# Optimization experiments

Measured on AMD Instinct MI355X. Metric: run time of the kernel, lower is better.

Reference implementation:

```python
import jax, jax.numpy as jnp
import numpy as np

N_NODES = 100000
N_EDGES = 3200000


def gcn_conv(x, W, b, row, col, n):
    # PyG GCNConv: add self-loops, symmetric normalization D^-1/2 (A+I) D^-1/2 (X W) + b
    xw = x @ W  # [N, out]
    loops = jnp.arange(n)
    row2 = jnp.concatenate([row, loops])
    col2 = jnp.concatenate([col, loops])
    deg = jax.ops.segment_sum(jnp.ones_like(col2, dtype=xw.dtype), col2, num_segments=n)
    dinv = jnp.where(deg > 0, jax.lax.rsqrt(deg), 0.0)
    norm = dinv[row2] * dinv[col2]  # [E+N]
    msg = xw[row2] * norm[:, None]  # gather + scale
    out = jax.ops.segment_sum(msg, col2, num_segments=n)  # scatter-add to targets
    return out + b


def setup_inputs() -> dict:
    key = jax.random.key(0)
    ks = jax.random.split(key, 9)
    x = jax.random.normal(ks[0], (N_NODES, 2), dtype=jnp.float32)
    edge_index = jax.random.randint(ks[1], (2, N_EDGES), 0, N_NODES, dtype=jnp.int64)
    edge_attr = jax.random.normal(ks[2], (N_EDGES, 1), dtype=jnp.float32)
    # params (glorot-ish scale)
    W1 = jax.random.normal(ks[3], (2, 16), dtype=jnp.float32) * (1.0 / np.sqrt(2))
    b1 = jnp.zeros((16,), dtype=jnp.float32)
    We = jax.random.normal(ks[4], (33, 4), dtype=jnp.float32) * (1.0 / np.sqrt(33))
    be = jnp.zeros((4,), dtype=jnp.float32)
    W2 = jax.random.normal(ks[5], (16, 2), dtype=jnp.float32) * (1.0 / np.sqrt(16))
    b2 = jnp.zeros((2,), dtype=jnp.float32)
    return {"x": x, "edge_index": edge_index, "edge_attr": edge_attr,
            "W1": W1, "b1": b1, "We": We, "be": be, "W2": W2, "b2": b2}


def reference(x, edge_index, edge_attr, W1, b1, We, be, W2, b2):
    row, col = edge_index[0], edge_index[1]
    n = x.shape[0]
    h = gcn_conv(x, W1, b1, row, col, n)  # [N, 16]
    # edge update: gather src/dst features, concat with edge_attr, Linear+ReLU
    e_in = jnp.concatenate([h[row], edge_attr, h[col]], axis=1)  # [E, 33]
    e_out = jax.nn.relu(e_in @ We + be)  # [E, 4]
    out_x = gcn_conv(h, W2, b2, row, col, n)  # [N, 2]
    return jax.nn.log_softmax(out_x, axis=1), jax.nn.log_softmax(e_out, axis=1)
```

## Files before the change

kernel.cpp:

```cpp
#include <hip/hip_runtime.h>


#define BLK 256
#define BLKP 1024
#define CH 12500
#define VIT ((CH + 4 * BLKP - 1) / (4 * BLKP))
#define BSH 7
#define BSZ 128
#define NBMAX 1024
#define PAD 16
#define S1 262144.0f
#define S2 65536.0f
#define BIAS 8388608

__global__ __launch_bounds__(BLKP) void k_hist(const int* __restrict__ col,
                                               int* __restrict__ gcount,
                                               int E, int NB) {
    __shared__ int hist[NBMAX];
    int t = threadIdx.x;
    if (t < NBMAX) hist[t] = 0;
    __syncthreads();
    int e0 = blockIdx.x * CH;
    int cnt = min(CH, E - e0);
    #pragma unroll
    for (int i = 0; i < VIT; i++) {
        int k = 4 * (t + i * BLKP);
        if (k + 3 < cnt) {
            int4 c = *reinterpret_cast<const int4*>(col + e0 + k);
            atomicAdd(&hist[c.x >> BSH], 1);
            atomicAdd(&hist[c.y >> BSH], 1);
            atomicAdd(&hist[c.z >> BSH], 1);
            atomicAdd(&hist[c.w >> BSH], 1);
        } else if (k < cnt) {
            for (int q = k; q < cnt; q++)
                atomicAdd(&hist[col[e0 + q] >> BSH], 1);
        }
    }
    __syncthreads();
    if (t < NB) {
        int h = hist[t];
        if (h) atomicAdd(&gcount[t * PAD], h);
    }
}

__global__ void k_scan(const int* __restrict__ gcount, int* __restrict__ gbase,
                       int* __restrict__ gcursor, int NB) {
    __shared__ int sa[NBMAX], sb[NBMAX];
    int t = threadIdx.x;
    for (int i = t; i < NBMAX; i += BLK) sa[i] = (i < NB) ? gcount[i * PAD] : 0;
    __syncthreads();
    int *src = sa, *dst = sb;
    for (int off = 1; off < NBMAX; off <<= 1) {
        for (int i = t; i < NBMAX; i += BLK)
            dst[i] = src[i] + ((i >= off) ? src[i - off] : 0);
        __syncthreads();
        int* tmp = src; src = dst; dst = tmp;
    }
    for (int i = t; i < NB; i += BLK) {
        int ex = src[i] - gcount[i * PAD];
        gbase[i] = ex;
        gcursor[i * PAD] = ex;
    }
    if (t == 0) gbase[NB] = src[NB - 1];
}

__global__ __launch_bounds__(BLKP) void k_part(const int* __restrict__ row,
                                               const int* __restrict__ col,
                                               int* __restrict__ gcursor,
                                               unsigned* __restrict__ part,
                                               int E, int NB) {
    __shared__ int hist[NBMAX];
    __shared__ int lstart[NBMAX];
    __shared__ int lcur[NBMAX];
    __shared__ int gb[NBMAX];
    __shared__ unsigned sbuf[CH];
    __shared__ unsigned short bid[CH];
    __shared__ int wsum[BLKP / 64];
    int t = threadIdx.x;
    int e0 = blockIdx.x * CH;
    int cnt = min(CH, E - e0);
    if (t < NBMAX) hist[t] = 0;
    __syncthreads();
    int4 cv[VIT];
    #pragma unroll
    for (int i = 0; i < VIT; i++) {
        int k = 4 * (t + i * BLKP);
        if (k + 3 < cnt) {
            int4 c = *reinterpret_cast<const int4*>(col + e0 + k);
            cv[i] = c;
            atomicAdd(&hist[c.x >> BSH], 1);
            atomicAdd(&hist[c.y >> BSH], 1);
            atomicAdd(&hist[c.z >> BSH], 1);
            atomicAdd(&hist[c.w >> BSH], 1);
        } else if (k < cnt) {
            int4 c = make_int4(0, 0, 0, 0);
            int m = cnt - k;
            c.x = col[e0 + k];             atomicAdd(&hist[c.x >> BSH], 1);
            if (m > 1) { c.y = col[e0 + k + 1]; atomicAdd(&hist[c.y >> BSH], 1); }
            if (m > 2) { c.z = col[e0 + k + 2]; atomicAdd(&hist[c.z >> BSH], 1); }
            cv[i] = c;
        }
    }
    __syncthreads();
    int h = hist[t];
    int lane = t & 63, wid = t >> 6;
    int v = h;
    #pragma unroll
    for (int off = 1; off < 64; off <<= 1) {
        int u = __shfl_up(v, off);
        if (lane >= off) v += u;
    }
    if (lane == 63) wsum[wid] = v;
    __syncthreads();
    int base = v - h;
    for (int w = 0; w < wid; w++) base += wsum[w];
    lstart[t] = base;
    lcur[t]   = base;
    gb[t] = h ? atomicAdd(&gcursor[t * PAD], h) : 0;
    __syncthreads();
    #pragma unroll
    for (int i = 0; i < VIT; i++) {
        int k = 4 * (t + i * BLKP);
        if (k + 3 < cnt) {
            int4 r = *reinterpret_cast<const int4*>(row + e0 + k);
            int4 c = cv[i];
            int b0 = c.x >> BSH, b1 = c.y >> BSH, b2 = c.z >> BSH, b3 = c.w >> BSH;
            int o0 = atomicAdd(&lcur[b0], 1);
            int o1 = atomicAdd(&lcur[b1], 1);
            int o2 = atomicAdd(&lcur[b2], 1);
            int o3 = atomicAdd(&lcur[b3], 1);
            sbuf[o0] = ((unsigned)r.x << BSH) | (unsigned)(c.x & (BSZ - 1));
            sbuf[o1] = ((unsigned)r.y << BSH) | (unsigned)(c.y & (BSZ - 1));
            sbuf[o2] = ((unsigned)r.z << BSH) | (unsigned)(c.z & (BSZ - 1));
            sbuf[o3] = ((unsigned)r.w << BSH) | (unsigned)(c.w & (BSZ - 1));
            bid[o0] = (unsigned short)b0;
            bid[o1] = (unsigned short)b1;
            bid[o2] = (unsigned short)b2;
            bid[o3] = (unsigned short)b3;
        } else if (k < cnt) {
            int m = cnt - k;
            int cs[3] = {cv[i].x, cv[i].y, cv[i].z};
            for (int q = 0; q < m && q < 3; q++) {
                int c = cs[q];
                int r = row[e0 + k + q];
                int b = c >> BSH;
                int off = atomicAdd(&lcur[b], 1);
                sbuf[off] = ((unsigned)r << BSH) | (unsigned)(c & (BSZ - 1));
                bid[off] = (unsigned short)b;
            }
        }
    }
    __syncthreads();
    for (int j = t; j < cnt; j += BLKP) {
        int b = bid[j];
        part[gb[b] + (j - lstart[b])] = sbuf[j];
    }
}

__global__ void k_nodeA(const unsigned* __restrict__ part, const int* __restrict__ gbase,
                        const float2* __restrict__ x2, float* __restrict__ dinv,
                        int* __restrict__ degi, int2* __restrict__ pi, int N) {
    __shared__ int cnt[BSZ];
    int t = threadIdx.x;
    if (t < BSZ) cnt[t] = 0;
    __syncthreads();
    int b = blockIdx.x;
    int j0 = gbase[b], j1 = gbase[b + 1];
    for (int j = j0 + 4 * t; j < j1; j += 4 * BLK) {
        int m = j1 - j;
        if (m >= 4) {
            unsigned w0 = part[j], w1 = part[j + 1], w2 = part[j + 2], w3 = part[j + 3];
            atomicAdd(&cnt[w0 & (BSZ - 1)], 1);
            atomicAdd(&cnt[w1 & (BSZ - 1)], 1);
            atomicAdd(&cnt[w2 & (BSZ - 1)], 1);
            atomicAdd(&cnt[w3 & (BSZ - 1)], 1);
        } else {
            for (int q = 0; q < m; q++)
                atomicAdd(&cnt[part[j + q] & (BSZ - 1)], 1);
        }
    }
    __syncthreads();
    if (t < BSZ) {
        int node = (b << BSH) + t;
        if (node < N) {
            int dg = cnt[t];
            degi[node] = dg;
            float d = rsqrtf((float)(dg + 1));
            dinv[node] = d;
            float2 xv = x2[node];
            pi[node] = make_int2(__float2int_rn(xv.x * d * S1),
                                 __float2int_rn(xv.y * d * S1));
        }
    }
}

__device__ __forceinline__ unsigned long long packi2(int2 p) {
    return ((unsigned long long)(unsigned)p.x << 32) | (unsigned)(p.y + BIAS);
}

__global__ void k_nodeB(const unsigned* __restrict__ part, const int* __restrict__ gbase,
                        const float* __restrict__ dinv, const int* __restrict__ degi,
                        const int2* __restrict__ pi,
                        const float* __restrict__ W1, const float* __restrict__ b1,
                        const float* __restrict__ W2, const float* __restrict__ We,
                        const float* __restrict__ be,
                        float4* __restrict__ U, float4* __restrict__ V,
                        int2* __restrict__ qi, int N) {
    __shared__ unsigned long long acc[BSZ];
    __shared__ float sW1[32], sb1[16], sW2[32], sWr[64], sWc[64], sbe[4];
    int t = threadIdx.x;
    if (t < BSZ) acc[t] = 0ull;
    if (t < 32) sW1[t] = W1[t];
    else if (t < 64) sW2[t - 32] = W2[t - 32];
    else if (t < 80) sb1[t - 64] = b1[t - 64];
    else if (t < 144) sWr[t - 80] = We[t - 80];
    else if (t < 208) sWc[t - 144] = We[68 + (t - 144)];
    else if (t < 212) sbe[t - 208] = be[t - 208];
    __syncthreads();
    int b = blockIdx.x;
    int j0 = gbase[b], j1 = gbase[b + 1];
    for (int j = j0 + 4 * t; j < j1; j += 4 * BLK) {
        int m = j1 - j;
        if (m >= 4) {
            unsigned w0 = part[j], w1 = part[j + 1], w2 = part[j + 2], w3 = part[j + 3];
            int2 p0 = pi[w0 >> BSH], p1 = pi[w1 >> BSH];
            int2 p2 = pi[w2 >> BSH], p3 = pi[w3 >> BSH];
            atomicAdd(&acc[w0 & (BSZ - 1)], packi2(p0));
            atomicAdd(&acc[w1 & (BSZ - 1)], packi2(p1));
            atomicAdd(&acc[w2 & (BSZ - 1)], packi2(p2));
            atomicAdd(&acc[w3 & (BSZ - 1)], packi2(p3));
        } else {
            for (int q = 0; q < m; q++) {
                unsigned w = part[j + q];
                atomicAdd(&acc[w & (BSZ - 1)], packi2(pi[w >> BSH]));
            }
        }
    }
    __syncthreads();
    if (t < BSZ) {
        int node = (b << BSH) + t;
        if (node < N) {
            unsigned long long a = acc[t];
            int sx = (int)(unsigned)(a >> 32);
            long long sy = (long long)(unsigned)(a & 0xffffffffull)
                         - (long long)degi[node] * BIAS;
            int2 ps = pi[node];
            float d = dinv[node];
            float ax = (float)(ps.x + (long long)sx) * (1.0f / S1);
            float ay = (float)(ps.y + sy) * (1.0f / S1);
            float s0 = d * ax, s1 = d * ay;
            float u0 = sbe[0], u1 = sbe[1], u2 = sbe[2], u3 = sbe[3];
            float v0 = 0.f, v1 = 0.f, v2 = 0.f, v3 = 0.f;
            float w0 = 0.f, w1 = 0.f;
            #pragma unroll
            for (int jj = 0; jj < 16; jj++) {
                float hj = fmaf(s0, sW1[jj], fmaf(s1, sW1[16 + jj], sb1[jj]));
                u0 = fmaf(hj, sWr[4 * jj + 0], u0);
                u1 = fmaf(hj, sWr[4 * jj + 1], u1);
                u2 = fmaf(hj, sWr[4 * jj + 2], u2);
                u3 = fmaf(hj, sWr[4 * jj + 3], u3);
                v0 = fmaf(hj, sWc[4 * jj + 0], v0);
                v1 = fmaf(hj, sWc[4 * jj + 1], v1);
                v2 = fmaf(hj, sWc[4 * jj + 2], v2);
                v3 = fmaf(hj, sWc[4 * jj + 3], v3);
                w0 = fmaf(hj, sW2[2 * jj], w0);
                w1 = fmaf(hj, sW2[2 * jj + 1], w1);
            }
            U[node] = make_float4(u0, u1, u2, u3);
            V[node] = make_float4(v0, v1, v2, v3);
            float qx = w0 * d, qy = w1 * d;
            qi[node] = make_int2(__float2int_rn(qx * S2), __float2int_rn(qy * S2));
        }
    }
}

__device__ __forceinline__ float4 edge_lsm(float4 u, float4 v, float av,
                                           const float* sW16) {
    float a0 = u.x + fmaf(av, sW16[0], v.x);
    float a1 = u.y + fmaf(av, sW16[1], v.y);
    float a2 = u.z + fmaf(av, sW16[2], v.z);
    float a3 = u.w + fmaf(av, sW16[3], v.w);
    a0 = fmaxf(a0, 0.f); a1 = fmaxf(a1, 0.f);
    a2 = fmaxf(a2, 0.f); a3 = fmaxf(a3, 0.f);
    float m = fmaxf(fmaxf(a0, a1), fmaxf(a2, a3));
    float s = expf(a0 - m) + expf(a1 - m) + expf(a2 - m) + expf(a3 - m);
    float l = m + logf(s);
    return make_float4(a0 - l, a1 - l, a2 - l, a3 - l);
}

__global__ void k_edge(const int* __restrict__ row, const int* __restrict__ col,
                       const float* __restrict__ ea, const float4* __restrict__ U,
                       const float4* __restrict__ V, const float* __restrict__ We,
                       float4* __restrict__ eout, int E) {
    __shared__ float sW16[4];
    int t = threadIdx.x;
    if (t < 4) sW16[t] = We[64 + t];
    __syncthreads();
    int base = blockIdx.x * (4 * BLK);
    int e0 = base + t;
    if (base + 4 * BLK <= E) {
        int r0 = row[e0], r1 = row[e0 + BLK], r2 = row[e0 + 2 * BLK], r3 = row[e0 + 3 * BLK];
        int c0 = col[e0], c1 = col[e0 + BLK], c2 = col[e0 + 2 * BLK], c3 = col[e0 + 3 * BLK];
        float a0 = ea[e0], a1 = ea[e0 + BLK], a2 = ea[e0 + 2 * BLK], a3 = ea[e0 + 3 * BLK];
        float4 u0 = U[r0], u1 = U[r1], u2 = U[r2], u3 = U[r3];
        float4 v0 = V[c0], v1 = V[c1], v2 = V[c2], v3 = V[c3];
        eout[e0]           = edge_lsm(u0, v0, a0, sW16);
        eout[e0 + BLK]     = edge_lsm(u1, v1, a1, sW16);
        eout[e0 + 2 * BLK] = edge_lsm(u2, v2, a2, sW16);
        eout[e0 + 3 * BLK] = edge_lsm(u3, v3, a3, sW16);
    } else {
        for (int q = 0; q < 4; q++) {
            int e = e0 + q * BLK;
            if (e < E)
                eout[e] = edge_lsm(U[row[e]], V[col[e]], ea[e], sW16);
        }
    }
}

__global__ void k_nodeC(const unsigned* __restrict__ part, const int* __restrict__ gbase,
                        const float* __restrict__ dinv, const int* __restrict__ degi,
                        const int2* __restrict__ qi,
                        const float* __restrict__ b2, float2* __restrict__ outn, int N) {
    __shared__ unsigned long long acc[BSZ];
    int t = threadIdx.x;
    if (t < BSZ) acc[t] = 0ull;
    __syncthreads();
    int b = blockIdx.x;
    int j0 = gbase[b], j1 = gbase[b + 1];
    for (int j = j0 + 4 * t; j < j1; j += 4 * BLK) {
        int m = j1 - j;
        if (m >= 4) {
            unsigned w0 = part[j], w1 = part[j + 1], w2 = part[j + 2], w3 = part[j + 3];
            int2 q0 = qi[w0 >> BSH], q1 = qi[w1 >> BSH];
            int2 q2 = qi[w2 >> BSH], q3 = qi[w3 >> BSH];
            atomicAdd(&acc[w0 & (BSZ - 1)], packi2(q0));
            atomicAdd(&acc[w1 & (BSZ - 1)], packi2(q1));
            atomicAdd(&acc[w2 & (BSZ - 1)], packi2(q2));
            atomicAdd(&acc[w3 & (BSZ - 1)], packi2(q3));
        } else {
            for (int q = 0; q < m; q++) {
                unsigned w = part[j + q];
                atomicAdd(&acc[w & (BSZ - 1)], packi2(qi[w >> BSH]));
            }
        }
    }
    __syncthreads();
    if (t < BSZ) {
        int node = (b << BSH) + t;
        if (node < N) {
            unsigned long long a = acc[t];
            int sx = (int)(unsigned)(a >> 32);
            long long sy = (long long)(unsigned)(a & 0xffffffffull)
                         - (long long)degi[node] * BIAS;
            int2 qs = qi[node];
            float d = dinv[node];
            float bx = (float)(qs.x + (long long)sx) * (1.0f / S2);
            float by = (float)(qs.y + sy) * (1.0f / S2);
            float o0 = fmaf(d, bx, b2[0]);
            float o1 = fmaf(d, by, b2[1]);
            float m = fmaxf(o0, o1);
            float l2 = m + logf(expf(o0 - m) + expf(o1 - m));
            outn[node] = make_float2(o0 - l2, o1 - l2);
        }
    }
}

extern "C" void kernel_launch(void* const* d_in, const int* in_sizes, int n_in,
                              void* d_out, int out_size, void* d_ws, size_t ws_size,
                              hipStream_t stream) {
    const float* x  = (const float*)d_in[0];
    const int*   ei = (const int*)d_in[1];
    const float* ea = (const float*)d_in[2];
    const float* W1 = (const float*)d_in[3];
    const float* b1 = (const float*)d_in[4];
    const float* We = (const float*)d_in[5];
    const float* be = (const float*)d_in[6];
    const float* W2 = (const float*)d_in[7];
    const float* b2 = (const float*)d_in[8];

    const int N = in_sizes[0] / 2;
    const int E = in_sizes[2];
    const int* row = ei;
    const int* col = ei + E;
    const int NB  = (N + BSZ - 1) >> BSH;
    const int NCH = (E + CH - 1) / CH;

    float2* out_nodes = (float2*)d_out;
    float4* out_edges = (float4*)((float*)d_out + 2 * (size_t)N);

    char* ws = (char*)d_ws;
    int*      gbase   = (int*)     (ws + 0);
    float*    dinv    = (float*)   (ws + 8192);
    int*      degi    = (int*)     (ws + 408192);
    int2*     pi      = (int2*)    (ws + 808192);
    int2*     qi      = (int2*)    (ws + 1608192);
    float4*   U       = (float4*)  (ws + 2408192);
    float4*   V       = (float4*)  (ws + 4008192);
    unsigned* part    = (unsigned*)(ws + 5608192);
    int*      gcount  = (int*)     (ws + 2408192);
    int*      gcursor = (int*)     (ws + 4008192);

    hipMemsetAsync(gcount, 0, NBMAX * PAD * sizeof(int), stream);
    k_hist <<<NCH, BLKP, 0, stream>>>(col, gcount, E, NB);
    k_scan <<<1,   BLK,  0, stream>>>(gcount, gbase, gcursor, NB);
    k_part <<<NCH, BLKP, 0, stream>>>(row, col, gcursor, part, E, NB);
    k_nodeA<<<NB,  BLK,  0, stream>>>(part, gbase, (const float2*)x, dinv, degi, pi, N);
    k_nodeB<<<NB,  BLK,  0, stream>>>(part, gbase, dinv, degi, pi, W1, b1, W2, We, be, U, V, qi, N);
    k_edge <<<(E + 4 * BLK - 1) / (4 * BLK), BLK, 0, stream>>>(row, col, ea, U, V, We, out_edges, E);
    k_nodeC<<<NB,  BLK,  0, stream>>>(part, gbase, dinv, degi, qi, b2, out_nodes, N);
}
```

Baseline: 233.3 us.

## Replace histogram+scan with fixed-capacity buckets and fuse edge and final node kernels

Drops the histogram pass, the single-block prefix scan and the memset by giving each destination bucket a fixed 8192-entry slot region. Each bucket's range is then its base plus its final atomic cursor. The edge-output kernel and the second aggregation kernel are merged into one launch, with the block index choosing the role. This saves one read of the column array plus launch overhead, at the cost of a larger, sparser partition buffer and overflow risk if any bucket exceeds the capacity.

```diff
diff --git a/kernel.cpp b/kernel.cpp
--- a/kernel.cpp
+++ b/kernel.cpp
@@ -9,59 +9,15 @@
 #define BSZ 128
 #define NBMAX 1024
 #define PAD 16
+#define CAP 8192
+#define CAPSH 13
 #define S1 262144.0f
 #define S2 65536.0f
 #define BIAS 8388608
 
-__global__ __launch_bounds__(BLKP) void k_hist(const int* __restrict__ col,
-                                               int* __restrict__ gcount,
-                                               int E, int NB) {
-    __shared__ int hist[NBMAX];
-    int t = threadIdx.x;
-    if (t < NBMAX) hist[t] = 0;
-    __syncthreads();
-    int e0 = blockIdx.x * CH;
-    int cnt = min(CH, E - e0);
-    #pragma unroll
-    for (int i = 0; i < VIT; i++) {
-        int k = 4 * (t + i * BLKP);
-        if (k + 3 < cnt) {
-            int4 c = *reinterpret_cast<const int4*>(col + e0 + k);
-            atomicAdd(&hist[c.x >> BSH], 1);
-            atomicAdd(&hist[c.y >> BSH], 1);
-            atomicAdd(&hist[c.z >> BSH], 1);
-            atomicAdd(&hist[c.w >> BSH], 1);
-        } else if (k < cnt) {
-            for (int q = k; q < cnt; q++)
-                atomicAdd(&hist[col[e0 + q] >> BSH], 1);
-        }
-    }
-    __syncthreads();
-    if (t < NB) {
-        int h = hist[t];
-        if (h) atomicAdd(&gcount[t * PAD], h);
-    }
-}
-
-__global__ void k_scan(const int* __restrict__ gcount, int* __restrict__ gbase,
-                       int* __restrict__ gcursor, int NB) {
-    __shared__ int sa[NBMAX], sb[NBMAX];
-    int t = threadIdx.x;
-    for (int i = t; i < NBMAX; i += BLK) sa[i] = (i < NB) ? gcount[i * PAD] : 0;
-    __syncthreads();
-    int *src = sa, *dst = sb;
-    for (int off = 1; off < NBMAX; off <<= 1) {
-        for (int i = t; i < NBMAX; i += BLK)
-            dst[i] = src[i] + ((i >= off) ? src[i - off] : 0);
-        __syncthreads();
-        int* tmp = src; src = dst; dst = tmp;
-    }
-    for (int i = t; i < NB; i += BLK) {
-        int ex = src[i] - gcount[i * PAD];
-        gbase[i] = ex;
-        gcursor[i * PAD] = ex;
-    }
-    if (t == 0) gbase[NB] = src[NB - 1];
+__global__ void k_init(int* __restrict__ gcursor, int NB) {
+    int t = threadIdx.x;
+    if (t < NB) gcursor[t * PAD] = t << CAPSH;
 }
 
 __global__ __launch_bounds__(BLKP) void k_part(const int* __restrict__ row,
@@ -157,7 +113,7 @@
     }
 }
 
-__global__ void k_nodeA(const unsigned* __restrict__ part, const int* __restrict__ gbase,
+__global__ void k_nodeA(const unsigned* __restrict__ part, const int* __restrict__ gcursor,
                         const float2* __restrict__ x2, float* __restrict__ dinv,
                         int* __restrict__ degi, int2* __restrict__ pi, int N) {
     __shared__ int cnt[BSZ];
@@ -165,7 +121,7 @@
     if (t < BSZ) cnt[t] = 0;
     __syncthreads();
     int b = blockIdx.x;
-    int j0 = gbase[b], j1 = gbase[b + 1];
+    int j0 = b << CAPSH, j1 = gcursor[b * PAD];
     for (int j = j0 + 4 * t; j < j1; j += 4 * BLK) {
         int m = j1 - j;
         if (m >= 4) {
@@ -198,7 +154,7 @@
     return ((unsigned long long)(unsigned)p.x << 32) | (unsigned)(p.y + BIAS);
 }
 
-__global__ void k_nodeB(const unsigned* __restrict__ part, const int* __restrict__ gbase,
+__global__ void k_nodeB(const unsigned* __restrict__ part, const int* __restrict__ gcursor,
                         const float* __restrict__ dinv, const int* __restrict__ degi,
                         const int2* __restrict__ pi,
                         const float* __restrict__ W1, const float* __restrict__ b1,
@@ -218,7 +174,7 @@
     else if (t < 212) sbe[t - 208] = be[t - 208];
     __syncthreads();
     int b = blockIdx.x;
-    int j0 = gbase[b], j1 = gbase[b + 1];
+    int j0 = b << CAPSH, j1 = gcursor[b * PAD];
     for (int j = j0 + 4 * t; j < j1; j += 4 * BLK) {
         int m = j1 - j;
         if (m >= 4) {
@@ -288,45 +244,45 @@
     return make_float4(a0 - l, a1 - l, a2 - l, a3 - l);
 }
 
-__global__ void k_edge(const int* __restrict__ row, const int* __restrict__ col,
+__global__ void k_tail(const int* __restrict__ row, const int* __restrict__ col,
                        const float* __restrict__ ea, const float4* __restrict__ U,
                        const float4* __restrict__ V, const float* __restrict__ We,
-                       float4* __restrict__ eout, int E) {
-    __shared__ float sW16[4];
-    int t = threadIdx.x;
-    if (t < 4) sW16[t] = We[64 + t];
-    __syncthreads();
-    int base = blockIdx.x * (4 * BLK);
-    int e0 = base + t;
-    if (base + 4 * BLK <= E) {
-        int r0 = row[e0], r1 = row[e0 + BLK], r2 = row[e0 + 2 * BLK], r3 = row[e0 + 3 * BLK];
-        int c0 = col[e0], c1 = col[e0 + BLK], c2 = col[e0 + 2 * BLK], c3 = col[e0 + 3 * BLK];
-        float a0 = ea[e0], a1 = ea[e0 + BLK], a2 = ea[e0 + 2 * BLK], a3 = ea[e0 + 3 * BLK];
-        float4 u0 = U[r0], u1 = U[r1], u2 = U[r2], u3 = U[r3];
-        float4 v0 = V[c0], v1 = V[c1], v2 = V[c2], v3 = V[c3];
-        eout[e0]           = edge_lsm(u0, v0, a0, sW16);
-        eout[e0 + BLK]     = edge_lsm(u1, v1, a1, sW16);
-        eout[e0 + 2 * BLK] = edge_lsm(u2, v2, a2, sW16);
-        eout[e0 + 3 * BLK] = edge_lsm(u3, v3, a3, sW16);
-    } else {
-        for (int q = 0; q < 4; q++) {
-            int e = e0 + q * BLK;
-            if (e < E)
-                eout[e] = edge_lsm(U[row[e]], V[col[e]], ea[e], sW16);
-        }
-    }
-}
-
-__global__ void k_nodeC(const unsigned* __restrict__ part, const int* __restrict__ gbase,
-                        const float* __restrict__ dinv, const int* __restrict__ degi,
-                        const int2* __restrict__ qi,
-                        const float* __restrict__ b2, float2* __restrict__ outn, int N) {
+                       float4* __restrict__ eout,
+                       const unsigned* __restrict__ part, const int* __restrict__ gcursor,
+                       const float* __restrict__ dinv, const int* __restrict__ degi,
+                       const int2* __restrict__ qi, const float* __restrict__ b2,
+                       float2* __restrict__ outn, int E, int N, int EB) {
     __shared__ unsigned long long acc[BSZ];
     int t = threadIdx.x;
+    if (blockIdx.x < (unsigned)EB) {
+        float* sW16 = (float*)acc;
+        if (t < 4) sW16[t] = We[64 + t];
+        __syncthreads();
+        int base = blockIdx.x * (4 * BLK);
+        int e0 = base + t;
+        if (base + 4 * BLK <= E) {
+            int r0 = row[e0], r1 = row[e0 + BLK], r2 = row[e0 + 2 * BLK], r3 = row[e0 + 3 * BLK];
+            int c0 = col[e0], c1 = col[e0 + BLK], c2 = col[e0 + 2 * BLK], c3 = col[e0 + 3 * BLK];
+            float a0 = ea[e0], a1 = ea[e0 + BLK], a2 = ea[e0 + 2 * BLK], a3 = ea[e0 + 3 * BLK];
+            float4 u0 = U[r0], u1 = U[r1], u2 = U[r2], u3 = U[r3];
+            float4 v0 = V[c0], v1 = V[c1], v2 = V[c2], v3 = V[c3];
+            eout[e0]           = edge_lsm(u0, v0, a0, sW16);
+            eout[e0 + BLK]     = edge_lsm(u1, v1, a1, sW16);
+            eout[e0 + 2 * BLK] = edge_lsm(u2, v2, a2, sW16);
+            eout[e0 + 3 * BLK] = edge_lsm(u3, v3, a3, sW16);
+        } else {
+            for (int q = 0; q < 4; q++) {
+                int e = e0 + q * BLK;
+                if (e < E)
+                    eout[e] = edge_lsm(U[row[e]], V[col[e]], ea[e], sW16);
+            }
+        }
+        return;
+    }
+    int b = blockIdx.x - EB;
     if (t < BSZ) acc[t] = 0ull;
     __syncthreads();
-    int b = blockIdx.x;
-    int j0 = gbase[b], j1 = gbase[b + 1];
+    int j0 = b << CAPSH, j1 = gcursor[b * PAD];
     for (int j = j0 + 4 * t; j < j1; j += 4 * BLK) {
         int m = j1 - j;
         if (m >= 4) {
@@ -384,28 +340,26 @@
     const int* col = ei + E;
     const int NB  = (N + BSZ - 1) >> BSH;
     const int NCH = (E + CH - 1) / CH;
+    const int EB  = (E + 4 * BLK - 1) / (4 * BLK);
 
     float2* out_nodes = (float2*)d_out;
     float4* out_edges = (float4*)((float*)d_out + 2 * (size_t)N);
 
     char* ws = (char*)d_ws;
-    int*      gbase   = (int*)     (ws + 0);
-    float*    dinv    = (float*)   (ws + 8192);
-    int*      degi    = (int*)     (ws + 408192);
-    int2*     pi      = (int2*)    (ws + 808192);
-    int2*     qi      = (int2*)    (ws + 1608192);
-    float4*   U       = (float4*)  (ws + 2408192);
-    float4*   V       = (float4*)  (ws + 4008192);
-    unsigned* part    = (unsigned*)(ws + 5608192);
-    int*      gcount  = (int*)     (ws + 2408192);
-    int*      gcursor = (int*)     (ws + 4008192);
-
-    hipMemsetAsync(gcount, 0, NBMAX * PAD * sizeof(int), stream);
-    k_hist <<<NCH, BLKP, 0, stream>>>(col, gcount, E, NB);
-    k_scan <<<1,   BLK,  0, stream>>>(gcount, gbase, gcursor, NB);
+    int*      gcursor = (int*)     (ws + 0);
+    float*    dinv    = (float*)   (ws + 65536);
+    int*      degi    = (int*)     (ws + 465536);
+    int2*     pi      = (int2*)    (ws + 865536);
+    int2*     qi      = (int2*)    (ws + 1665536);
+    float4*   U       = (float4*)  (ws + 2465536);
+    float4*   V       = (float4*)  (ws + 4065536);
+    unsigned* part    = (unsigned*)(ws + 5665536);
+
+    k_init <<<1,   BLKP, 0, stream>>>(gcursor, NB);
     k_part <<<NCH, BLKP, 0, stream>>>(row, col, gcursor, part, E, NB);
-    k_nodeA<<<NB,  BLK,  0, stream>>>(part, gbase, (const float2*)x, dinv, degi, pi, N);
-    k_nodeB<<<NB,  BLK,  0, stream>>>(part, gbase, dinv, degi, pi, W1, b1, W2, We, be, U, V, qi, N);
-    k_edge <<<(E + 4 * BLK - 1) / (4 * BLK), BLK, 0, stream>>>(row, col, ea, U, V, We, out_edges, E);
-    k_nodeC<<<NB,  BLK,  0, stream>>>(part, gbase, dinv, degi, qi, b2, out_nodes, N);
-}
+    k_nodeA<<<NB,  BLK,  0, stream>>>(part, gcursor, (const float2*)x, dinv, degi, pi, N);
+    k_nodeB<<<NB,  BLK,  0, stream>>>(part, gcursor, dinv, degi, pi, W1, b1, W2, We, be, U, V, qi, N);
+    k_tail <<<EB + NB, BLK, 0, stream>>>(row, col, ea, U, V, We, out_edges,
+                                         part, gcursor, dinv, degi, qi, b2,
+                                         out_nodes, E, N, EB);
+}
```

Result: faster. 204.1 us (median of 2 runs) (-12.5%).
